# Optimization experiments

Measured on AMD Instinct MI355X. Metric: run time of the kernel, lower is better.

The kernel has to match this reference:

```python
import jax, jax.numpy as jnp
import numpy as np

N = 50000   # nodes
E = 800000  # edges
D = 256     # in = hidden = out channels
R = 16      # num_relations (last index reserved for self-loops)
B = 8       # num_bases
LN_EPS = 1e-5


def setup_inputs() -> dict:
    key = jax.random.key(0)
    ks = jax.random.split(key, 20)
    s_basis = np.sqrt(2.0 / (D + D)).astype(np.float32)  # glorot-ish scale
    s_att = np.sqrt(2.0 / (R + B)).astype(np.float32)
    inp = {
        "x": jax.random.normal(ks[0], (N, D), dtype=jnp.float32),
        "edge_index": jax.random.randint(ks[1], (2, E), 0, N),
        "edge_type": jax.random.randint(ks[2], (E,), 0, R),
        "edge_attr": jax.random.uniform(ks[3], (E,), dtype=jnp.float32),
        # layer 1 params
        "basis1": jax.random.normal(ks[4], (B, D, D), dtype=jnp.float32) * s_basis,
        "att1": jax.random.normal(ks[5], (R, B), dtype=jnp.float32) * s_att,
        "root1": jax.random.normal(ks[6], (D, D), dtype=jnp.float32) * s_basis,
        "bias1": jnp.zeros((D,), dtype=jnp.float32),
        "ln1_g": jnp.ones((D,), dtype=jnp.float32),
        "ln1_b": jnp.zeros((D,), dtype=jnp.float32),
        # layer 2 params
        "basis2": jax.random.normal(ks[7], (B, D, D), dtype=jnp.float32) * s_basis,
        "att2": jax.random.normal(ks[8], (R, B), dtype=jnp.float32) * s_att,
        "root2": jax.random.normal(ks[9], (D, D), dtype=jnp.float32) * s_basis,
        "bias2": jnp.zeros((D,), dtype=jnp.float32),
        "ln2_g": jnp.ones((D,), dtype=jnp.float32),
        "ln2_b": jnp.zeros((D,), dtype=jnp.float32),
    }
    return inp


def _layer_norm(x, g, b):
    mu = jnp.mean(x, axis=-1, keepdims=True)
    var = jnp.mean(jnp.square(x - mu), axis=-1, keepdims=True)
    return (x - mu) * jax.lax.rsqrt(var + LN_EPS) * g + b


def _rgcn_layer(x, edge_index, edge_type, edge_attr, basis, att, root, bias):
    n = x.shape[0]
    r = att.shape[0]
    # W_r = sum_b a_rb V_b ; then per-relation transform of every node.
    weight = jnp.einsum('rb,bio->rio', att, basis)          # [R, D, D]
    H = jnp.einsum('ni,rio->nro', x, weight)                # [N, R, D]
    # append self-loops with relation index R-1 and confidence 1.0
    loop = jnp.arange(n, dtype=edge_index.dtype)
    src = jnp.concatenate([edge_index[0], loop])
    dst = jnp.concatenate([edge_index[1], loop])
    et = jnp.concatenate([edge_type, jnp.full((n,), r - 1, dtype=edge_type.dtype)])
    ea = jnp.concatenate([edge_attr, jnp.ones((n,), dtype=x.dtype)])
    msg = H[src, et] * ea[:, None]                          # [E+N, D]
    summ = jax.ops.segment_sum(msg, dst, num_segments=n)
    cnt = jax.ops.segment_sum(jnp.ones_like(ea), dst, num_segments=n)
    agg = summ / cnt[:, None]                               # scatter-mean (cnt >= 1 via self-loops)
    return agg + x @ root + bias


def reference(x, edge_index, edge_type, edge_attr,
              basis1, att1, root1, bias1, ln1_g, ln1_b,
              basis2, att2, root2, bias2, ln2_g, ln2_b):
    # input_proj / output_proj are Identity since in == hidden == out.
    h = x
    h_out = _rgcn_layer(h, edge_index, edge_type, edge_attr, basis1, att1, root1, bias1)
    h = jax.nn.relu(_layer_norm(h + h_out, ln1_g, ln1_b))
    h_out = _rgcn_layer(h, edge_index, edge_type, edge_attr, basis2, att2, root2, bias2)
    h = jax.nn.relu(_layer_norm(h + h_out, ln2_g, ln2_b))
    return h
```

## Files before the change

### kernel.cpp

```cpp
#include <hip/hip_runtime.h>
#include <stdint.h>

#define D 256
#define RREL 16
#define BB 8
#define K9 2304
#define LN_EPS 1e-5f
#define NT (K9 / 64)

typedef __attribute__((ext_vector_type(8))) short frag8;
typedef __attribute__((ext_vector_type(4))) float floatx4;
typedef __attribute__((ext_vector_type(2))) float float2v;

__device__ __forceinline__ unsigned short f2bf(float f) {
    union { float f; uint32_t u; } v; v.f = f;
    uint32_t r = (v.u + 0x7FFFu + ((v.u >> 16) & 1u)) >> 16;
    return (unsigned short)r;
}
__device__ __forceinline__ float bf2f(unsigned short u) {
    union { uint32_t u; float f; } v; v.u = (uint32_t)u << 16;
    return v.f;
}
__device__ __forceinline__ float2v bfpair(uint32_t d) {
    union { uint32_t u; float f; } lo, hi;
    lo.u = d << 16; hi.u = d & 0xFFFF0000u;
    return (float2v){lo.f, hi.f};
}

__device__ __forceinline__ float2v pk_mul(float2v a, float2v b) {
    float2v d;
    asm("v_pk_mul_f32 %0, %1, %2" : "=v"(d) : "v"(a), "v"(b));
    return d;
}
__device__ __forceinline__ void pk_fma_lo(float2v& acc, float2v c, float2v x) {
    asm("v_pk_fma_f32 %0, %1, %2, %0 op_sel:[0,0,0] op_sel_hi:[1,0,1]"
        : "+v"(acc) : "v"(c), "v"(x));
}
__device__ __forceinline__ void pk_fma_hi(float2v& acc, float2v c, float2v x) {
    asm("v_pk_fma_f32 %0, %1, %2, %0 op_sel:[0,1,0] op_sel_hi:[1,1,1]"
        : "+v"(acc) : "v"(c), "v"(x));
}

__device__ __forceinline__ void gl2lds16(const unsigned short* g, char* l) {
    __builtin_amdgcn_global_load_lds((const __attribute__((address_space(1))) void*)g,
                                     (__attribute__((address_space(3))) void*)l, 16, 0, 0);
}

__global__ __launch_bounds__(256) void k_cvt(const float* __restrict__ src,
                                             unsigned short* __restrict__ dst, int n4) {
    int i = blockIdx.x * 256 + threadIdx.x;
    if (i >= n4) return;
    float4 v = ((const float4*)src)[i];
    ushort4 o = make_ushort4(f2bf(v.x), f2bf(v.y), f2bf(v.z), f2bf(v.w));
    ((ushort4*)dst)[i] = o;
}

__global__ void k_deg(const int* __restrict__ ei, int* __restrict__ deg, int E) {
    int e = blockIdx.x * 256 + threadIdx.x;
    if (e < E) atomicAdd(&deg[ei[E + e]], 1);
}

__global__ __launch_bounds__(256) void k_scan1(const int* __restrict__ deg,
                                               int* __restrict__ csum, int N) {
    __shared__ int sh[256];
    int n = blockIdx.x * 256 + threadIdx.x;
    sh[threadIdx.x] = (n < N) ? deg[n] : 0;
    __syncthreads();
    for (int off = 128; off > 0; off >>= 1) {
        if (threadIdx.x < off) sh[threadIdx.x] += sh[threadIdx.x + off];
        __syncthreads();
    }
    if (threadIdx.x == 0) csum[blockIdx.x] = sh[0];
}

__global__ __launch_bounds__(256) void k_scan2(int* __restrict__ csum, int nch,
                                               int* __restrict__ rowptr, int N) {
    __shared__ int sh[256];
    int tid = threadIdx.x;
    if (nch <= 256) {
        int v = (tid < nch) ? csum[tid] : 0;
        sh[tid] = v;
        __syncthreads();
        for (int off = 1; off < 256; off <<= 1) {
            int t = (tid >= off) ? sh[tid - off] : 0;
            __syncthreads();
            sh[tid] += t;
            __syncthreads();
        }
        if (tid < nch) csum[tid] = sh[tid] - v;
        if (tid == 255) rowptr[N] = sh[255];
    } else if (tid == 0) {
        int s = 0;
        for (int i = 0; i < nch; ++i) { int c = csum[i]; csum[i] = s; s += c; }
        rowptr[N] = s;
    }
}

__global__ __launch_bounds__(256) void k_scan3(const int* __restrict__ deg,
                                               const int* __restrict__ csum,
                                               int* __restrict__ rowptr,
                                               int* __restrict__ cursor,
                                               float* __restrict__ cnt, int N) {
    __shared__ int sh[256];
    int tid = threadIdx.x;
    int n = blockIdx.x * 256 + tid;
    int v = (n < N) ? deg[n] : 0;
    sh[tid] = v;
    __syncthreads();
    for (int off = 1; off < 256; off <<= 1) {
        int t = (tid >= off) ? sh[tid - off] : 0;
        __syncthreads();
        sh[tid] += t;
        __syncthreads();
    }
    int excl = sh[tid] - v + csum[blockIdx.x];
    if (n < N) {
        rowptr[n] = excl;
        cursor[n] = excl;
        cnt[n] = (float)(v + 1);
    }
}

__global__ void k_scatter(const int* __restrict__ ei, const int* __restrict__ et,
                          const float* __restrict__ ea, int* __restrict__ cursor,
                          int2* __restrict__ ep, int E) {
    int e = blockIdx.x * 256 + threadIdx.x;
    if (e >= E) return;
    int dst = ei[E + e];
    int p = atomicAdd(&cursor[dst], 1);
    ep[p] = make_int2(ei[e] | (et[e] << 24), __float_as_int(ea[e]));
}

__global__ __launch_bounds__(256) void k_prep_w(const float* __restrict__ basis,
                                                const float* __restrict__ root,
                                                unsigned short* __restrict__ Wt) {
    __shared__ float tile[64][65];
    int k0 = blockIdx.x * 64, o0 = blockIdx.y * 64;
    const float* src = (k0 < BB * D) ? (basis + (size_t)k0 * D)
                                     : (root + (size_t)(k0 - BB * D) * D);
    int tid = threadIdx.x;
#pragma unroll
    for (int t = 0; t < 16; ++t) {
        int idx = t * 256 + tid;
        int kk = idx >> 6, oo = idx & 63;
        tile[kk][oo] = src[(size_t)kk * D + o0 + oo];
    }
    __syncthreads();
#pragma unroll
    for (int t = 0; t < 16; ++t) {
        int idx = t * 256 + tid;
        int oo = idx >> 6, kk = idx & 63;
        Wt[(size_t)(o0 + oo) * K9 + k0 + kk] = f2bf(tile[kk][oo]);
    }
}

__device__ __forceinline__ void edge_fma(float2v g2[4][4], float2v c0, float2v c1,
                                         float2v c2, float2v c3,
                                         float2v x0, float2v x1) {
    pk_fma_lo(g2[0][0], c0, x0); pk_fma_lo(g2[1][0], c1, x0);
    pk_fma_lo(g2[2][0], c2, x0); pk_fma_lo(g2[3][0], c3, x0);
    pk_fma_hi(g2[0][1], c0, x0); pk_fma_hi(g2[1][1], c1, x0);
    pk_fma_hi(g2[2][1], c2, x0); pk_fma_hi(g2[3][1], c3, x0);
    pk_fma_lo(g2[0][2], c0, x1); pk_fma_lo(g2[1][2], c1, x1);
    pk_fma_lo(g2[2][2], c2, x1); pk_fma_lo(g2[3][2], c3, x1);
    pk_fma_hi(g2[0][3], c0, x1); pk_fma_hi(g2[1][3], c1, x1);
    pk_fma_hi(g2[2][3], c2, x1); pk_fma_hi(g2[3][3], c3, x1);
}

__global__ __launch_bounds__(256) void k_gather(
    const unsigned short* __restrict__ xb, const float* __restrict__ att,
    const int* __restrict__ rowptr, const int2* __restrict__ ep,
    const float* __restrict__ cnt, unsigned short* __restrict__ G,
    int n0, int rows, int N) {
    __shared__ __align__(32) float att_s[RREL * BB];
    int tid = threadIdx.x;
    if (tid < RREL * BB) att_s[tid] = att[tid];
    __syncthreads();
    int wv = tid >> 6, lane = tid & 63;
    int rloc = blockIdx.x * 4 + wv;
    if (rloc >= rows) return;
    int n = n0 + rloc;
    unsigned short* gout = G + (size_t)rloc * K9 + lane * 4;
    if (n >= N) {
        ushort4 z = make_ushort4(0, 0, 0, 0);
#pragma unroll
        for (int b = 0; b <= BB; ++b) *(ushort4*)(gout + b * D) = z;
        return;
    }
    uint2 xu = *(const uint2*)&xb[(size_t)n * D + lane * 4];
    float2v xs0 = bfpair(xu.x), xs1 = bfpair(xu.y);
    float xv[4] = {xs0.x, xs0.y, xs1.x, xs1.y};

    float2v g2[4][4];
#pragma unroll
    for (int bp = 0; bp < 4; ++bp) {
        float2v ap = {att_s[(RREL - 1) * BB + 2 * bp],
                      att_s[(RREL - 1) * BB + 2 * bp + 1]};
#pragma unroll
        for (int j = 0; j < 4; ++j) {
            float2v xs = {xv[j], xv[j]};
            g2[bp][j] = ap * xs;
        }
    }

    int e0 = rowptr[n], e1 = rowptr[n + 1];
    int e = e0;
    for (; e + 2 <= e1; e += 2) {
        int2 pa = ep[e], pb = ep[e + 1];
        uint2 udA = *(const uint2*)&xb[(size_t)(pa.x & 0xFFFFFF) * D + lane * 4];
        uint2 udB = *(const uint2*)&xb[(size_t)(pb.x & 0xFFFFFF) * D + lane * 4];
        int ra = (unsigned)pa.x >> 24, rb = (unsigned)pb.x >> 24;
        const float4* Ar = (const float4*)&att_s[ra * BB];
        const float4* Br = (const float4*)&att_s[rb * BB];
        float4 a0 = Ar[0], a1 = Ar[1];
        float4 b0 = Br[0], b1 = Br[1];
        float wa = __int_as_float(pa.y);
        float2v wa2 = {wa, wa};
        float2v ca0 = pk_mul(wa2, (float2v){a0.x, a0.y});
        float2v ca1 = pk_mul(wa2, (float2v){a0.z, a0.w});
        float2v ca2 = pk_mul(wa2, (float2v){a1.x, a1.y});
        float2v ca3 = pk_mul(wa2, (float2v){a1.z, a1.w});
        float2v xA0 = bfpair(udA.x), xA1 = bfpair(udA.y);
        edge_fma(g2, ca0, ca1, ca2, ca3, xA0, xA1);
        float wb = __int_as_float(pb.y);
        float2v wb2 = {wb, wb};
        float2v cb0 = pk_mul(wb2, (float2v){b0.x, b0.y});
        float2v cb1 = pk_mul(wb2, (float2v){b0.z, b0.w});
        float2v cb2 = pk_mul(wb2, (float2v){b1.x, b1.y});
        float2v cb3 = pk_mul(wb2, (float2v){b1.z, b1.w});
        float2v xB0 = bfpair(udB.x), xB1 = bfpair(udB.y);
        edge_fma(g2, cb0, cb1, cb2, cb3, xB0, xB1);
    }
    if (e < e1) {
        int2 pa = ep[e];
        uint2 udA = *(const uint2*)&xb[(size_t)(pa.x & 0xFFFFFF) * D + lane * 4];
        int ra = (unsigned)pa.x >> 24;
        const float4* Ar = (const float4*)&att_s[ra * BB];
        float4 a0 = Ar[0], a1 = Ar[1];
        float wa = __int_as_float(pa.y);
        float2v wa2 = {wa, wa};
        float2v ca0 = pk_mul(wa2, (float2v){a0.x, a0.y});
        float2v ca1 = pk_mul(wa2, (float2v){a0.z, a0.w});
        float2v ca2 = pk_mul(wa2, (float2v){a1.x, a1.y});
        float2v ca3 = pk_mul(wa2, (float2v){a1.z, a1.w});
        float2v xA0 = bfpair(udA.x), xA1 = bfpair(udA.y);
        edge_fma(g2, ca0, ca1, ca2, ca3, xA0, xA1);
    }
#pragma unroll
    for (int bp = 0; bp < 4; ++bp) {
        ushort4 o0 = make_ushort4(f2bf(g2[bp][0].x), f2bf(g2[bp][1].x),
                                  f2bf(g2[bp][2].x), f2bf(g2[bp][3].x));
        *(ushort4*)(gout + (2 * bp) * D) = o0;
        ushort4 o1 = make_ushort4(f2bf(g2[bp][0].y), f2bf(g2[bp][1].y),
                                  f2bf(g2[bp][2].y), f2bf(g2[bp][3].y));
        *(ushort4*)(gout + (2 * bp + 1) * D) = o1;
    }
    float cn = cnt[n];
    ushort4 o = make_ushort4(f2bf(cn * xv[0]), f2bf(cn * xv[1]),
                             f2bf(cn * xv[2]), f2bf(cn * xv[3]));
    *(ushort4*)(gout + BB * D) = o;
}

__global__ __launch_bounds__(512, 4) void k_gemm(
    const unsigned short* __restrict__ G, const unsigned short* __restrict__ Wt,
    const float* __restrict__ hin, const float* __restrict__ cnt,
    const float* __restrict__ bias, const float* __restrict__ gln,
    const float* __restrict__ bln, float* __restrict__ hout,
    unsigned short* __restrict__ houtb, int n0, int N) {
    __shared__ __align__(16) char smem[40960];
    char* Asb = smem;
    char* Bsb = smem + 8192;
    float* ps   = (float*)smem;
    float* pq   = ps + 256;
    float* mu_s = ps + 512;
    float* rs_s = ps + 576;

    int tid = threadIdx.x;
    int wv = tid >> 6, lane = tid & 63;
    int quad = lane >> 4, l16 = lane & 15;
    int wm = wv >> 2, wn = wv & 3;
    int grow = blockIdx.x * 64;
    int nb = n0 + grow;

    int arow_s = tid >> 3, aslot_s = tid & 7;
    const unsigned short* gA =
        G + (size_t)(grow + arow_s) * K9 + ((aslot_s ^ (arow_s & 7)) << 3);
    char* lA = Asb + (tid << 4);
    const unsigned short* gB[4]; char* lB[4];
#pragma unroll
    for (int t = 0; t < 4; ++t) {
        int c = t * 512 + tid;
        int brow = c >> 3, bslot = c & 7;
        gB[t] = Wt + (size_t)brow * K9 + ((bslot ^ (brow & 7)) << 3);
        lB[t] = Bsb + (c << 4);
    }

    floatx4 acc[2][4];
#pragma unroll
    for (int mf = 0; mf < 2; ++mf)
#pragma unroll
        for (int nf = 0; nf < 4; ++nf) acc[mf][nf] = (floatx4){0.f, 0.f, 0.f, 0.f};

    for (int it = 0; it < NT; ++it) {
        __syncthreads();
        int koff = it * 64;
        gl2lds16(gA + koff, lA);
#pragma unroll
        for (int t = 0; t < 4; ++t) gl2lds16(gB[t] + koff, lB[t]);
        __syncthreads();
#pragma unroll
        for (int kc = 0; kc < 2; ++kc) {
            int g = kc * 4 + quad;
            frag8 a[2], b[4];
#pragma unroll
            for (int mf = 0; mf < 2; ++mf) {
                int arow = wm * 32 + mf * 16 + l16;
                a[mf] = *(const frag8*)(Asb + arow * 128 + ((g ^ (arow & 7)) << 4));
            }
#pragma unroll
            for (int nf = 0; nf < 4; ++nf) {
                int brow = wn * 64 + nf * 16 + l16;
                b[nf] = *(const frag8*)(Bsb + brow * 128 + ((g ^ (brow & 7)) << 4));
            }
#pragma unroll
            for (int mf = 0; mf < 2; ++mf)
#pragma unroll
                for (int nf = 0; nf < 4; ++nf)
                    acc[mf][nf] = __builtin_amdgcn_mfma_f32_16x16x32_bf16(
                        a[mf], b[nf], acc[mf][nf], 0, 0, 0);
        }
    }
    __syncthreads();

    int col[4]; float bic[4];
#pragma unroll
    for (int nf = 0; nf < 4; ++nf) {
        col[nf] = wn * 64 + nf * 16 + l16;
        bic[nf] = bias[col[nf]];
    }
#pragma unroll
    for (int mf = 0; mf < 2; ++mf) {
#pragma unroll
        for (int r = 0; r < 4; ++r) {
            int row = wm * 32 + mf * 16 + quad * 4 + r;
            int n = nb + row;
            float s = 0.f, sq = 0.f;
            if (n < N) {
                float inv = 1.0f / cnt[n];
                const float* hp = hin + (size_t)n * D;
#pragma unroll
                for (int nf = 0; nf < 4; ++nf) {
                    float v = acc[mf][nf][r] * inv + hp[col[nf]] + bic[nf];
                    acc[mf][nf][r] = v;
                    s += v; sq += v * v;
                }
            }
            s += __shfl_xor(s, 1); sq += __shfl_xor(sq, 1);
            s += __shfl_xor(s, 2); sq += __shfl_xor(sq, 2);
            s += __shfl_xor(s, 4); sq += __shfl_xor(sq, 4);
            s += __shfl_xor(s, 8); sq += __shfl_xor(sq, 8);
            if (l16 == 0) {
                ps[row * 4 + wn] = s;
                pq[row * 4 + wn] = sq;
            }
        }
    }
    __syncthreads();
    if (tid < 64) {
        float s  = ps[tid * 4] + ps[tid * 4 + 1] + ps[tid * 4 + 2] + ps[tid * 4 + 3];
        float sq = pq[tid * 4] + pq[tid * 4 + 1] + pq[tid * 4 + 2] + pq[tid * 4 + 3];
        float mu = s * (1.f / D);
        mu_s[tid] = mu;
        rs_s[tid] = rsqrtf(sq * (1.f / D) - mu * mu + LN_EPS);
    }
    __syncthreads();

    float gc[4], bc[4];
#pragma unroll
    for (int nf = 0; nf < 4; ++nf) {
        gc[nf] = gln[col[nf]];
        bc[nf] = bln[col[nf]];
    }
#pragma unroll
    for (int mf = 0; mf < 2; ++mf) {
#pragma unroll
        for (int r = 0; r < 4; ++r) {
            int row = wm * 32 + mf * 16 + quad * 4 + r;
            int n = nb + row;
            if (n >= N) continue;
            float mu = mu_s[row], rs = rs_s[row];
            float* op = hout + (size_t)n * D;
#pragma unroll
            for (int nf = 0; nf < 4; ++nf) {
                float o = fmaxf((acc[mf][nf][r] - mu) * rs * gc[nf] + bc[nf], 0.f);
                op[col[nf]] = o;
                if (houtb) houtb[(size_t)n * D + col[nf]] = f2bf(o);
            }
        }
    }
}

extern "C" void kernel_launch(void* const* d_in, const int* in_sizes, int n_in,
                              void* d_out, int out_size, void* d_ws, size_t ws_size,
                              hipStream_t stream) {
    const float* x      = (const float*)d_in[0];
    const int*   ei     = (const int*)d_in[1];
    const int*   et     = (const int*)d_in[2];
    const float* ea     = (const float*)d_in[3];
    const float* basis1 = (const float*)d_in[4];
    const float* att1   = (const float*)d_in[5];
    const float* root1  = (const float*)d_in[6];
    const float* bias1  = (const float*)d_in[7];
    const float* g1     = (const float*)d_in[8];
    const float* b1     = (const float*)d_in[9];
    const float* basis2 = (const float*)d_in[10];
    const float* att2   = (const float*)d_in[11];
    const float* root2  = (const float*)d_in[12];
    const float* bias2  = (const float*)d_in[13];
    const float* g2     = (const float*)d_in[14];
    const float* b2     = (const float*)d_in[15];
    float* out = (float*)d_out;

    int N = in_sizes[0] / D;
    int E = in_sizes[2];
    int nch = (N + 255) / 256;
    int Mp = ((N + 63) / 64) * 64;
    int T = Mp / 64;

    char* p = (char*)d_ws;
    size_t used = 0;
    auto alloc = [&](size_t bytes) {
        char* q = p;
        size_t a = (bytes + 255) & ~(size_t)255;
        p += a; used += a;
        return q;
    };
    float*          h1     = (float*)alloc((size_t)N * D * 4);
    unsigned short* xb     = (unsigned short*)alloc((size_t)N * D * 2);
    unsigned short* h1b    = (unsigned short*)alloc((size_t)N * D * 2);
    unsigned short* Wt     = (unsigned short*)alloc((size_t)K9 * D * 2);
    int*            deg    = (int*)alloc((size_t)N * 4);
    int*            rowptr = (int*)alloc((size_t)(N + 1) * 4);
    int*            cursor = (int*)alloc((size_t)N * 4);
    float*          cnt    = (float*)alloc((size_t)N * 4);
    int2*           ep     = (int2*)alloc((size_t)E * 8);
    int*            csum   = (int*)alloc((size_t)nch * 4);
    size_t remain = (ws_size > used + 256) ? (ws_size - used - 256) : 0;
    size_t tile_bytes = (size_t)64 * K9 * 2;
    int ct = (int)(remain / tile_bytes);
    if (ct < 1) ct = 1;
    if (ct > T) ct = T;
    unsigned short* G = (unsigned short*)alloc((size_t)ct * tile_bytes);

    hipMemsetAsync(deg, 0, (size_t)N * 4, stream);
    int gE = (E + 255) / 256;
    k_deg<<<gE, 256, 0, stream>>>(ei, deg, E);
    k_scan1<<<nch, 256, 0, stream>>>(deg, csum, N);
    k_scan2<<<1, 256, 0, stream>>>(csum, nch, rowptr, N);
    k_scan3<<<nch, 256, 0, stream>>>(deg, csum, rowptr, cursor, cnt, N);
    k_scatter<<<gE, 256, 0, stream>>>(ei, et, ea, cursor, ep, E);
    k_cvt<<<(N * D / 4 + 255) / 256, 256, 0, stream>>>(x, xb, N * D / 4);

    const float* bas[2]  = {basis1, basis2};
    const float* attp[2] = {att1, att2};
    const float* rt[2]   = {root1, root2};
    const float* bi[2]   = {bias1, bias2};
    const float* lg[2]   = {g1, g2};
    const float* lb[2]   = {b1, b2};
    const unsigned short* gin[2] = {xb, h1b};
    const float* hres[2] = {x, h1};
    float*          hof[2] = {h1, out};
    unsigned short* hob[2] = {h1b, nullptr};

    for (int L = 0; L < 2; ++L) {
        k_prep_w<<<dim3(K9 / 64, D / 64), 256, 0, stream>>>(bas[L], rt[L], Wt);
        for (int c0 = 0; c0 < T; c0 += ct) {
            int tiles = (T - c0 < ct) ? (T - c0) : ct;
            int rows = tiles * 64;
            int n0 = c0 * 64;
            k_gather<<<rows / 4, 256, 0, stream>>>(gin[L], attp[L], rowptr, ep,
                                                   cnt, G, n0, rows, N);
            k_gemm<<<tiles, 512, 0, stream>>>(G, Wt, hres[L], cnt, bi[L], lg[L], lb[L],
                                              hof[L], hob[L], n0, N);
        }
    }
}
```

Measured before the change: 739.0 us.

## Double-buffer GEMM LDS tiles and double block M-tile to 128 rows

The GEMM kernel now uses 1024-thread blocks covering 128 rows each, so every loaded B (weight) tile is reused across twice as many rows. It also replaces the single-buffered load/compute loop with a two-stage LDS double buffer, issuing the next K-slice while MFMAs consume the current one and halving the barriers per step. Host chunking pads the tile count to an even number to fit the 128-row blocks. LDS per block grows to 96KB, which limits occupancy to one block per CU, and the larger blocks mean fewer blocks in the grid.

```diff
diff --git a/kernel.cpp b/kernel.cpp
--- a/kernel.cpp
+++ b/kernel.cpp
@@ -7,6 +7,7 @@
 #define K9 2304
 #define LN_EPS 1e-5f
 #define NT (K9 / 64)
+#define BUFB 49152
 
 typedef __attribute__((ext_vector_type(8))) short frag8;
 typedef __attribute__((ext_vector_type(4))) float floatx4;
@@ -261,38 +262,36 @@
     *(ushort4*)(gout + BB * D) = o;
 }
 
-__global__ __launch_bounds__(512, 4) void k_gemm(
+__global__ __launch_bounds__(1024, 4) void k_gemm(
     const unsigned short* __restrict__ G, const unsigned short* __restrict__ Wt,
     const float* __restrict__ hin, const float* __restrict__ cnt,
     const float* __restrict__ bias, const float* __restrict__ gln,
     const float* __restrict__ bln, float* __restrict__ hout,
     unsigned short* __restrict__ houtb, int n0, int N) {
-    __shared__ __align__(16) char smem[40960];
-    char* Asb = smem;
-    char* Bsb = smem + 8192;
+    __shared__ __align__(16) char smem[2 * BUFB];
     float* ps   = (float*)smem;
-    float* pq   = ps + 256;
-    float* mu_s = ps + 512;
-    float* rs_s = ps + 576;
+    float* pq   = ps + 512;
+    float* mu_s = ps + 1024;
+    float* rs_s = ps + 1152;
 
     int tid = threadIdx.x;
     int wv = tid >> 6, lane = tid & 63;
     int quad = lane >> 4, l16 = lane & 15;
     int wm = wv >> 2, wn = wv & 3;
-    int grow = blockIdx.x * 64;
+    int grow = blockIdx.x * 128;
     int nb = n0 + grow;
 
     int arow_s = tid >> 3, aslot_s = tid & 7;
     const unsigned short* gA =
         G + (size_t)(grow + arow_s) * K9 + ((aslot_s ^ (arow_s & 7)) << 3);
-    char* lA = Asb + (tid << 4);
-    const unsigned short* gB[4]; char* lB[4];
-#pragma unroll
-    for (int t = 0; t < 4; ++t) {
-        int c = t * 512 + tid;
+    char* lA = smem + (tid << 4);
+    const unsigned short* gB[2]; char* lB[2];
+#pragma unroll
+    for (int t = 0; t < 2; ++t) {
+        int c = t * 1024 + tid;
         int brow = c >> 3, bslot = c & 7;
         gB[t] = Wt + (size_t)brow * K9 + ((bslot ^ (brow & 7)) << 3);
-        lB[t] = Bsb + (c << 4);
+        lB[t] = smem + 16384 + (c << 4);
     }
 
     floatx4 acc[2][4];
@@ -301,13 +300,15 @@
 #pragma unroll
         for (int nf = 0; nf < 4; ++nf) acc[mf][nf] = (floatx4){0.f, 0.f, 0.f, 0.f};
 
-    for (int it = 0; it < NT; ++it) {
-        __syncthreads();
+    auto STAGE = [&](int it, int soff) {
         int koff = it * 64;
-        gl2lds16(gA + koff, lA);
-#pragma unroll
-        for (int t = 0; t < 4; ++t) gl2lds16(gB[t] + koff, lB[t]);
-        __syncthreads();
+        gl2lds16(gA + koff, lA + soff);
+        gl2lds16(gB[0] + koff, lB[0] + soff);
+        gl2lds16(gB[1] + koff, lB[1] + soff);
+    };
+    auto COMPUTE = [&](int soff) {
+        const char* Ab = smem + soff;
+        const char* Bb = Ab + 16384;
 #pragma unroll
         for (int kc = 0; kc < 2; ++kc) {
             int g = kc * 4 + quad;
@@ -315,12 +316,12 @@
 #pragma unroll
             for (int mf = 0; mf < 2; ++mf) {
                 int arow = wm * 32 + mf * 16 + l16;
-                a[mf] = *(const frag8*)(Asb + arow * 128 + ((g ^ (arow & 7)) << 4));
+                a[mf] = *(const frag8*)(Ab + arow * 128 + ((g ^ (arow & 7)) << 4));
             }
 #pragma unroll
             for (int nf = 0; nf < 4; ++nf) {
                 int brow = wn * 64 + nf * 16 + l16;
-                b[nf] = *(const frag8*)(Bsb + brow * 128 + ((g ^ (brow & 7)) << 4));
+                b[nf] = *(const frag8*)(Bb + brow * 128 + ((g ^ (brow & 7)) << 4));
             }
 #pragma unroll
             for (int mf = 0; mf < 2; ++mf)
@@ -329,8 +330,18 @@
                     acc[mf][nf] = __builtin_amdgcn_mfma_f32_16x16x32_bf16(
                         a[mf], b[nf], acc[mf][nf], 0, 0, 0);
         }
-    }
-    __syncthreads();
+    };
+
+    STAGE(0, 0);
+    __syncthreads();
+    for (int it = 0; it < NT; it += 2) {
+        STAGE(it + 1, BUFB);
+        COMPUTE(0);
+        __syncthreads();
+        if (it + 2 < NT) STAGE(it + 2, 0);
+        COMPUTE(BUFB);
+        __syncthreads();
+    }
 
     int col[4]; float bic[4];
 #pragma unroll
@@ -366,7 +377,7 @@
         }
     }
     __syncthreads();
-    if (tid < 64) {
+    if (tid < 128) {
         float s  = ps[tid * 4] + ps[tid * 4 + 1] + ps[tid * 4 + 2] + ps[tid * 4 + 3];
         float sq = pq[tid * 4] + pq[tid * 4 + 1] + pq[tid * 4 + 2] + pq[tid * 4 + 3];
         float mu = s * (1.f / D);
@@ -426,6 +437,7 @@
     int nch = (N + 255) / 256;
     int Mp = ((N + 63) / 64) * 64;
     int T = Mp / 64;
+    int Tpad = (T + 1) & ~1;
 
     char* p = (char*)d_ws;
     size_t used = 0;
@@ -447,10 +459,16 @@
     int*            csum   = (int*)alloc((size_t)nch * 4);
     size_t remain = (ws_size > used + 256) ? (ws_size - used - 256) : 0;
     size_t tile_bytes = (size_t)64 * K9 * 2;
-    int ct = (int)(remain / tile_bytes);
-    if (ct < 1) ct = 1;
-    if (ct > T) ct = T;
-    unsigned short* G = (unsigned short*)alloc((size_t)ct * tile_bytes);
+    int ct_max = (int)(remain / tile_bytes);
+    if (ct_max < 2) ct_max = 2;
+    if (ct_max > Tpad) ct_max = Tpad;
+    unsigned short* G = (unsigned short*)alloc((size_t)ct_max * tile_bytes);
+
+    int nch2 = (Tpad + ct_max - 1) / ct_max;
+    int ct = (Tpad + nch2 - 1) / nch2;
+    ct = (ct + 1) & ~1;
+    if (ct > ct_max) ct = ct_max & ~1;
+    if (ct < 2) ct = 2;
 
     hipMemsetAsync(deg, 0, (size_t)N * 4, stream);
     int gE = (E + 255) / 256;
@@ -474,14 +492,15 @@
 
     for (int L = 0; L < 2; ++L) {
         k_prep_w<<<dim3(K9 / 64, D / 64), 256, 0, stream>>>(bas[L], rt[L], Wt);
-        for (int c0 = 0; c0 < T; c0 += ct) {
-            int tiles = (T - c0 < ct) ? (T - c0) : ct;
+        for (int c0 = 0; c0 < Tpad; c0 += ct) {
+            int tiles = (Tpad - c0 < ct) ? (Tpad - c0) : ct;
             int rows = tiles * 64;
             int n0 = c0 * 64;
             k_gather<<<rows / 4, 256, 0, stream>>>(gin[L], attp[L], rowptr, ep,
                                                    cnt, G, n0, rows, N);
-            k_gemm<<<tiles, 512, 0, stream>>>(G, Wt, hres[L], cnt, bi[L], lg[L], lb[L],
-                                              hof[L], hob[L], n0, N);
+            k_gemm<<<rows / 128, 1024, 0, stream>>>(G, Wt, hres[L], cnt, bi[L],
+                                                    lg[L], lb[L], hof[L], hob[L],
+                                                    n0, N);
         }
     }
 }
```

After: 626.3 us. 1.18x faster.
